# Performance work log

Hardware: AMD Instinct MI355X
Metric: run time of the kernel (lower is better)

## Reference

```python
import jax, jax.numpy as jnp
import numpy as np

HIDDEN = 512
TEXT_DIM = 768
NUM_HEADS = 8
NUM_GROUPS = 32
GN_EPS = 1e-5
COS_EPS = 1e-6


def setup_inputs() -> dict:
    key = jax.random.key(0)
    ks = jax.random.split(key, 9)
    s = 0.02
    return {
        "x": jax.random.normal(ks[0], (16, HIDDEN, 64, 64), jnp.float32),
        "text_emb": jax.random.normal(ks[1], (16, 77, TEXT_DIM), jnp.float32),
        "gn_weight": jnp.ones((HIDDEN,), jnp.float32),
        "gn_bias": jnp.zeros((HIDDEN,), jnp.float32),
        "Wq": jax.random.normal(ks[2], (HIDDEN, HIDDEN), jnp.float32) * s,
        "Wk": jax.random.normal(ks[3], (HIDDEN, TEXT_DIM), jnp.float32) * s,
        "Wv": jax.random.normal(ks[4], (HIDDEN, TEXT_DIM), jnp.float32) * s,
        "Wo": jax.random.normal(ks[5], (HIDDEN, HIDDEN), jnp.float32) * s,
        "bo": jnp.zeros((HIDDEN,), jnp.float32),
    }


def reference(x, text_emb, gn_weight, gn_bias, Wq, Wk, Wv, Wo, bo):
    B, C, H, W = x.shape
    N_img = H * W
    nh, hd = NUM_HEADS, C // NUM_HEADS

    # GroupNorm(32, C): normalize over (channels-in-group, H, W)
    xg = x.reshape(B, NUM_GROUPS, -1)
    mu = xg.mean(axis=-1, keepdims=True)
    var = jnp.mean(jnp.square(xg - mu), axis=-1, keepdims=True)
    xn = ((xg - mu) * jax.lax.rsqrt(var + GN_EPS)).reshape(B, C, H, W)
    xn = xn * gn_weight[None, :, None, None] + gn_bias[None, :, None, None]

    x_flat = xn.reshape(B, C, N_img).transpose(0, 2, 1)  # [B, N_img, C]

    q = jnp.einsum('bnc,dc->bnd', x_flat, Wq)            # [B, N_img, C]
    k = jnp.einsum('btc,dc->btd', text_emb, Wk)          # [B, N_text, C]
    v = jnp.einsum('btc,dc->btd', text_emb, Wv)

    # split heads -> [B, nh, N, hd]
    q = q.reshape(B, N_img, nh, hd).transpose(0, 2, 1, 3)
    k = k.reshape(B, -1, nh, hd).transpose(0, 2, 1, 3)
    v = v.reshape(B, -1, nh, hd).transpose(0, 2, 1, 3)

    # cosine-sim attention: L2-normalize q and k, scale = 1.0
    q = q / (jnp.linalg.norm(q, axis=-1, keepdims=True) + COS_EPS)
    k = k / (jnp.linalg.norm(k, axis=-1, keepdims=True) + COS_EPS)

    scores = jnp.einsum('bhqd,bhkd->bhqk', q, k)         # [B, nh, N_img, N_text]
    attn = jax.nn.softmax(scores, axis=-1)
    out = jnp.einsum('bhqk,bhkd->bhqd', attn, v)         # [B, nh, N_img, hd]

    out = out.transpose(0, 2, 1, 3).reshape(B, N_img, C)
    out = jnp.einsum('bnc,dc->bnd', out, Wo) + bo
    out = out.transpose(0, 2, 1).reshape(B, C, H, W)
    return x + out
```

## Files before the change

### kernel.cpp

```cpp
#include <hip/hip_runtime.h>
#include <math.h>


typedef unsigned short u16;
typedef __attribute__((ext_vector_type(8))) __bf16 bf16x8;
typedef __attribute__((ext_vector_type(4))) float f32x4;

typedef __attribute__((address_space(1))) unsigned int as1_u32;
typedef __attribute__((address_space(3))) unsigned int as3_u32;

__device__ __forceinline__ float b2f(u16 u) {
  union { unsigned int i; float f; } c; c.i = ((unsigned int)u) << 16; return c.f;
}
__device__ __forceinline__ u16 f2b(float f) {
  union { float f; unsigned int i; } c; c.f = f;
  unsigned int i = c.i + 0x7fffu + ((c.i >> 16) & 1u);
  return (u16)(i >> 16);
}

__device__ __forceinline__ void g2lds16(const void* g, void* l) {
  __builtin_amdgcn_global_load_lds((const as1_u32*)g, (as3_u32*)l, 16, 0, 0);
}

__global__ void k_castall(const float* __restrict__ Wq, const float* __restrict__ Wk,
                          const float* __restrict__ Wv, const float* __restrict__ Wo,
                          const float* __restrict__ text,
                          u16* __restrict__ wq_b, u16* __restrict__ wkv_b,
                          u16* __restrict__ wo_b, u16* __restrict__ text_b) {
  const int i = blockIdx.x * 256 + threadIdx.x, st = gridDim.x * 256;
  for (int j = i; j < 262144; j += st) wq_b[j] = f2b(Wq[j]);
  for (int j = i; j < 393216; j += st) wkv_b[j] = f2b(Wk[j]);
  for (int j = i; j < 393216; j += st) wkv_b[393216 + j] = f2b(Wv[j]);
  for (int j = i; j < 262144; j += st) wo_b[j] = f2b(Wo[j]);
  for (int j = i; j < 946176; j += st) text_b[j] = f2b(text[j]);
}

__global__ __launch_bounds__(256) void k_gnstats(const float* __restrict__ x,
                                                 float* __restrict__ stats) {
  int bg = blockIdx.x;
  const float4* p = (const float4*)(x + (size_t)bg * 65536);
  float s = 0.f, ss = 0.f;
  for (int i = threadIdx.x; i < 16384; i += 256) {
    float4 v = p[i];
    s  += v.x + v.y + v.z + v.w;
    ss += v.x*v.x + v.y*v.y + v.z*v.z + v.w*v.w;
  }
  for (int o = 1; o < 64; o <<= 1) { s += __shfl_xor(s, o, 64); ss += __shfl_xor(ss, o, 64); }
  __shared__ float as_[4], bs_[4];
  int w = threadIdx.x >> 6;
  if ((threadIdx.x & 63) == 0) { as_[w] = s; bs_[w] = ss; }
  __syncthreads();
  if (threadIdx.x == 0) {
    s  = as_[0] + as_[1] + as_[2] + as_[3];
    ss = bs_[0] + bs_[1] + bs_[2] + bs_[3];
    float mu  = s * (1.f / 65536.f);
    float var = ss * (1.f / 65536.f) - mu * mu;
    stats[2*bg]   = mu;
    stats[2*bg+1] = rsqrtf(var + 1e-5f);
  }
}

__global__ __launch_bounds__(256) void k_qproj(
    const float* __restrict__ x, const float* __restrict__ stats,
    const float* __restrict__ gw, const float* __restrict__ gb,
    const u16* __restrict__ Wqb, u16* __restrict__ qb) {
  __shared__ u16 Al[128 * 64];
  __shared__ u16 Bl[128 * 64];
  __shared__ float cw[512], cb[512];
  const int tid = threadIdx.x;
  const int o = blockIdx.x;
  const int mi = ((o >> 5) << 3) + (o & 7);
  const int ni = (o >> 3) & 3;
  const int m0 = mi << 7, n0 = ni << 7;
  const int b = m0 >> 12, hw0 = m0 & 4095;

  for (int c = tid; c < 512; c += 256) {
    const int g = (b << 5) + (c >> 4);
    const float mu = stats[2*g], rs = stats[2*g+1];
    const float wg = gw[c] * rs;
    cw[c] = wg; cb[c] = gb[c] - mu * wg;
  }

  const int l = tid & 63, w = tid >> 6;
  const int wm = (w >> 1) << 6, wn = (w & 1) << 6;
  const int lr = l & 15, lg = l >> 4;

  f32x4 acc[4][4];
#pragma unroll
  for (int i = 0; i < 4; ++i)
#pragma unroll
    for (int j = 0; j < 4; ++j) acc[i][j] = {0.f, 0.f, 0.f, 0.f};

  const int rl = l >> 3, slot = l & 7;
  const int c8 = (slot ^ rl) << 3;
  int brow[4];
#pragma unroll
  for (int j = 0; j < 4; ++j) brow[j] = n0 + (w << 5) + (j << 3) + rl;

  const int tokl = tid & 127;
  const int chg = tid >> 7;
  const float* xb = x + (((size_t)b) << 9) * 4096;
  __syncthreads();

  for (int ks = 0; ks < 8; ++ks) {
#pragma unroll
    for (int j = 0; j < 4; ++j)
      g2lds16(Wqb + (size_t)brow[j] * 512 + (ks << 6) + c8,
              Bl + (((w << 5) + (j << 3)) << 6));
#pragma unroll
    for (int jj = 0; jj < 8; ++jj) {
      const int ch4 = (((chg << 3) + jj) << 2);
      const int c = (ks << 6) + ch4;
      const float v0 = xb[(size_t)(c + 0) * 4096 + hw0 + tokl];
      const float v1 = xb[(size_t)(c + 1) * 4096 + hw0 + tokl];
      const float v2 = xb[(size_t)(c + 2) * 4096 + hw0 + tokl];
      const float v3 = xb[(size_t)(c + 3) * 4096 + hw0 + tokl];
      ushort4 pk;
      pk.x = f2b(v0 * cw[c + 0] + cb[c + 0]);
      pk.y = f2b(v1 * cw[c + 1] + cb[c + 1]);
      pk.z = f2b(v2 * cw[c + 2] + cb[c + 2]);
      pk.w = f2b(v3 * cw[c + 3] + cb[c + 3]);
      const int sl = (((ch4 >> 3) ^ (tokl & 7)) << 3) + (ch4 & 7);
      *(ushort4*)(Al + (tokl << 6) + sl) = pk;
    }
    __syncthreads();
    bf16x8 bfr[4][2];
#pragma unroll
    for (int j = 0; j < 4; ++j) {
      const int br = wn + j * 16 + lr;
      bfr[j][0] = *(const bf16x8*)(Bl + (br << 6) + (((lg    ) ^ (br & 7)) << 3));
      bfr[j][1] = *(const bf16x8*)(Bl + (br << 6) + (((lg + 4) ^ (br & 7)) << 3));
    }
#pragma unroll
    for (int i = 0; i < 4; ++i) {
      const int ar = wm + i * 16 + lr;
      const bf16x8 a0 = *(const bf16x8*)(Al + (ar << 6) + (((lg    ) ^ (ar & 7)) << 3));
      const bf16x8 a1 = *(const bf16x8*)(Al + (ar << 6) + (((lg + 4) ^ (ar & 7)) << 3));
#pragma unroll
      for (int j = 0; j < 4; ++j) {
        acc[i][j] = __builtin_amdgcn_mfma_f32_16x16x32_bf16(a0, bfr[j][0], acc[i][j], 0, 0, 0);
        acc[i][j] = __builtin_amdgcn_mfma_f32_16x16x32_bf16(a1, bfr[j][1], acc[i][j], 0, 0, 0);
      }
    }
    __syncthreads();
  }

  const int lg4 = lg << 2;
#pragma unroll
  for (int i = 0; i < 4; ++i) {
#pragma unroll
    for (int r = 0; r < 4; ++r) {
      float ss = 0.f;
#pragma unroll
      for (int j = 0; j < 4; ++j) { const float v = acc[i][j][r]; ss += v * v; }
      ss += __shfl_xor(ss, 1, 64); ss += __shfl_xor(ss, 2, 64);
      ss += __shfl_xor(ss, 4, 64); ss += __shfl_xor(ss, 8, 64);
      const float sc = 1.f / (sqrtf(ss) + 1e-6f);
      const int row = m0 + wm + i * 16 + lg4 + r;
#pragma unroll
      for (int j = 0; j < 4; ++j)
        qb[(size_t)row * 512 + n0 + wn + j * 16 + lr] = f2b(acc[i][j][r] * sc);
    }
  }
}

template <int MODE>
__global__ __launch_bounds__(256) void k_gemm(
    const u16* __restrict__ A, const u16* __restrict__ BT,
    int M, int N, int K,
    float* __restrict__ outf, u16* __restrict__ outb,
    const float* __restrict__ xres, const float* __restrict__ bias) {
  __shared__ u16 Al[2][128 * 64];
  __shared__ u16 Bl[2][128 * 64];
  const int tid = threadIdx.x;
  const int l = tid & 63, w = tid >> 6;

  const int nwg = gridDim.x * gridDim.y;
  int lin = blockIdx.y * gridDim.x + blockIdx.x;
  lin = (lin & 7) * (nwg >> 3) + (lin >> 3);
  const int m0 = (lin / gridDim.x) << 7, n0 = (lin % gridDim.x) << 7;

  const int wm = (w >> 1) << 6, wn = (w & 1) << 6;
  const int lr = l & 15, lg = l >> 4;

  f32x4 acc[4][4];
#pragma unroll
  for (int i = 0; i < 4; ++i)
#pragma unroll
    for (int j = 0; j < 4; ++j) acc[i][j] = {0.f, 0.f, 0.f, 0.f};

  const int rl = l >> 3, slot = l & 7;
  const int c8 = (slot ^ rl) << 3;
  int arow[4], brow[4];
#pragma unroll
  for (int j = 0; j < 4; ++j) {
    const int r_local = (w << 5) + (j << 3) + rl;
    arow[j] = min(m0 + r_local, M - 1);
    brow[j] = n0 + r_local;
  }

  const int ksteps = K >> 6;
#pragma unroll
  for (int j = 0; j < 4; ++j)
    g2lds16(A + (size_t)arow[j] * K + c8, Al[0] + (((w << 5) + (j << 3)) << 6));
#pragma unroll
  for (int j = 0; j < 4; ++j)
    g2lds16(BT + (size_t)brow[j] * K + c8, Bl[0] + (((w << 5) + (j << 3)) << 6));
  __syncthreads();

  for (int ks = 0; ks < ksteps; ++ks) {
    const int cur = ks & 1, nxt = cur ^ 1;
    if (ks + 1 < ksteps) {
      const int kb = ((ks + 1) << 6) + c8;
#pragma unroll
      for (int j = 0; j < 4; ++j)
        g2lds16(A + (size_t)arow[j] * K + kb, Al[nxt] + (((w << 5) + (j << 3)) << 6));
#pragma unroll
      for (int j = 0; j < 4; ++j)
        g2lds16(BT + (size_t)brow[j] * K + kb, Bl[nxt] + (((w << 5) + (j << 3)) << 6));
    }
    bf16x8 bfr[4][2];
#pragma unroll
    for (int j = 0; j < 4; ++j) {
      const int br = wn + j * 16 + lr;
      bfr[j][0] = *(const bf16x8*)(Bl[cur] + (br << 6) + (((lg    ) ^ (br & 7)) << 3));
      bfr[j][1] = *(const bf16x8*)(Bl[cur] + (br << 6) + (((lg + 4) ^ (br & 7)) << 3));
    }
#pragma unroll
    for (int i = 0; i < 4; ++i) {
      const int ar = wm + i * 16 + lr;
      const bf16x8 a0 = *(const bf16x8*)(Al[cur] + (ar << 6) + (((lg    ) ^ (ar & 7)) << 3));
      const bf16x8 a1 = *(const bf16x8*)(Al[cur] + (ar << 6) + (((lg + 4) ^ (ar & 7)) << 3));
#pragma unroll
      for (int j = 0; j < 4; ++j) {
        acc[i][j] = __builtin_amdgcn_mfma_f32_16x16x32_bf16(a0, bfr[j][0], acc[i][j], 0, 0, 0);
        acc[i][j] = __builtin_amdgcn_mfma_f32_16x16x32_bf16(a1, bfr[j][1], acc[i][j], 0, 0, 0);
      }
    }
    __syncthreads();
  }

  const int lg4 = lg << 2;
#pragma unroll
  for (int i = 0; i < 4; ++i) {
#pragma unroll
    for (int j = 0; j < 4; ++j) {
#pragma unroll
      for (int r = 0; r < 4; ++r) {
        const int row = m0 + wm + i * 16 + lg4 + r;
        const int col = n0 + wn + j * 16 + lr;
        const float v = acc[i][j][r];
        if (MODE == 0) {
          if (row < M) outf[(size_t)row * N + col] = v;
        } else {
          const int bb = col >> 12, hw = col & 4095;
          const size_t o = (((size_t)bb << 9) + row) * 4096 + hw;
          outf[o] = xres[o] + bias[row] + v;
        }
      }
    }
  }
}

__global__ __launch_bounds__(64) void k_kvnorm(const float* __restrict__ kv,
                                               u16* __restrict__ kn,
                                               u16* __restrict__ vn) {
  const int row = blockIdx.x;
  const int h = blockIdx.y;
  const int d = threadIdx.x;
  const int b = row / 77, t = row - b * 77;
  const float kx = kv[(size_t)row * 1024 + h * 64 + d];
  float ss = kx * kx;
  for (int o = 1; o < 64; o <<= 1) ss += __shfl_xor(ss, o, 64);
  const float sc = 1.f / (sqrtf(ss) + 1e-6f);
  const size_t ob = (((size_t)(b * 8 + h)) * 77 + t) * 64 + d;
  kn[ob] = f2b(kx * sc);
  vn[ob] = f2b(kv[(size_t)row * 1024 + 512 + h * 64 + d]);
}

__global__ __launch_bounds__(256) void k_attn2(
    const u16* __restrict__ q, const u16* __restrict__ kn,
    const u16* __restrict__ vn, u16* __restrict__ out) {
  __shared__ u16 Kl[96 * 72];
  __shared__ u16 Vt[64 * 104];
  __shared__ u16 Pl[64 * 104];
  const int qt = blockIdx.x, h = blockIdx.y, b = blockIdx.z;
  const size_t kvb = ((size_t)(b * 8 + h)) * (77 * 64);
  const int tid = threadIdx.x;
  for (int u = tid; u < 768; u += 256) {
    const int row = u >> 3, c8v = (u & 7) << 3;
    uint4 v = make_uint4(0, 0, 0, 0);
    if (row < 77) v = *(const uint4*)(kn + kvb + row * 64 + c8v);
    *(uint4*)(Kl + row * 72 + c8v) = v;
  }
  for (int u = tid; u < 768; u += 256) {
    const int row = u >> 3, c8v = (u & 7) << 3;
    uint4 v = make_uint4(0, 0, 0, 0);
    if (row < 77) v = *(const uint4*)(vn + kvb + row * 64 + c8v);
    const u16* pv = (const u16*)&v;
#pragma unroll
    for (int j = 0; j < 8; ++j) Vt[(c8v + j) * 104 + row] = pv[j];
  }
  __syncthreads();
  const int l = tid & 63, w = tid >> 6;
  const int lr = l & 15, lg = l >> 4;

  const int qrow = (b << 12) + (qt << 6) + (w << 4) + lr;
  bf16x8 af0 = *(const bf16x8*)(q + (size_t)qrow * 512 + h * 64 + lg * 8);
  bf16x8 af1 = *(const bf16x8*)(q + (size_t)qrow * 512 + h * 64 + 32 + lg * 8);
  f32x4 s[6];
#pragma unroll
  for (int nt = 0; nt < 6; ++nt) {
    s[nt] = {0.f, 0.f, 0.f, 0.f};
    bf16x8 bk0 = *(const bf16x8*)(Kl + (nt * 16 + lr) * 72 + lg * 8);
    bf16x8 bk1 = *(const bf16x8*)(Kl + (nt * 16 + lr) * 72 + 32 + lg * 8);
    s[nt] = __builtin_amdgcn_mfma_f32_16x16x32_bf16(af0, bk0, s[nt], 0, 0, 0);
    s[nt] = __builtin_amdgcn_mfma_f32_16x16x32_bf16(af1, bk1, s[nt], 0, 0, 0);
  }
#pragma unroll
  for (int r = 0; r < 4; ++r) {
    if (lr >= 13) s[4][r] = -1e30f;
    s[5][r] = -1e30f;
  }
#pragma unroll
  for (int r = 0; r < 4; ++r) {
    float m = s[0][r];
#pragma unroll
    for (int nt = 1; nt < 6; ++nt) m = fmaxf(m, s[nt][r]);
    m = fmaxf(m, __shfl_xor(m, 1, 64)); m = fmaxf(m, __shfl_xor(m, 2, 64));
    m = fmaxf(m, __shfl_xor(m, 4, 64)); m = fmaxf(m, __shfl_xor(m, 8, 64));
    float sum = 0.f;
#pragma unroll
    for (int nt = 0; nt < 6; ++nt) { s[nt][r] = __expf(s[nt][r] - m); sum += s[nt][r]; }
    sum += __shfl_xor(sum, 1, 64); sum += __shfl_xor(sum, 2, 64);
    sum += __shfl_xor(sum, 4, 64); sum += __shfl_xor(sum, 8, 64);
    const float inv = 1.f / sum;
    const int qlocal = (w << 4) + (lg << 2) + r;
#pragma unroll
    for (int nt = 0; nt < 6; ++nt)
      Pl[qlocal * 104 + nt * 16 + lr] = f2b(s[nt][r] * inv);
  }
  __syncthreads();

  bf16x8 pa0 = *(const bf16x8*)(Pl + ((w << 4) + lr) * 104 + lg * 8);
  bf16x8 pa1 = *(const bf16x8*)(Pl + ((w << 4) + lr) * 104 + 32 + lg * 8);
  bf16x8 pa2 = *(const bf16x8*)(Pl + ((w << 4) + lr) * 104 + 64 + lg * 8);
  f32x4 o[4];
#pragma unroll
  for (int nt = 0; nt < 4; ++nt) {
    o[nt] = {0.f, 0.f, 0.f, 0.f};
    bf16x8 bv0 = *(const bf16x8*)(Vt + (nt * 16 + lr) * 104 + lg * 8);
    bf16x8 bv1 = *(const bf16x8*)(Vt + (nt * 16 + lr) * 104 + 32 + lg * 8);
    bf16x8 bv2 = *(const bf16x8*)(Vt + (nt * 16 + lr) * 104 + 64 + lg * 8);
    o[nt] = __builtin_amdgcn_mfma_f32_16x16x32_bf16(pa0, bv0, o[nt], 0, 0, 0);
    o[nt] = __builtin_amdgcn_mfma_f32_16x16x32_bf16(pa1, bv1, o[nt], 0, 0, 0);
    o[nt] = __builtin_amdgcn_mfma_f32_16x16x32_bf16(pa2, bv2, o[nt], 0, 0, 0);
  }
#pragma unroll
  for (int r = 0; r < 4; ++r) {
    const int n = (b << 12) + (qt << 6) + (w << 4) + (lg << 2) + r;
#pragma unroll
    for (int nt = 0; nt < 4; ++nt)
      out[(size_t)n * 512 + h * 64 + nt * 16 + lr] = f2b(o[nt][r]);
  }
}

extern "C" void kernel_launch(void* const* d_in, const int* in_sizes, int n_in,
                              void* d_out, int out_size, void* d_ws, size_t ws_size,
                              hipStream_t stream) {
  (void)in_sizes; (void)n_in; (void)out_size; (void)ws_size;
  const float* x    = (const float*)d_in[0];
  const float* text = (const float*)d_in[1];
  const float* gnw  = (const float*)d_in[2];
  const float* gnb  = (const float*)d_in[3];
  const float* Wq   = (const float*)d_in[4];
  const float* Wk   = (const float*)d_in[5];
  const float* Wv   = (const float*)d_in[6];
  const float* Wo   = (const float*)d_in[7];
  const float* bo   = (const float*)d_in[8];
  float* out = (float*)d_out;

  char* ws = (char*)d_ws;
  size_t off = 0;
  auto alloc = [&](size_t bytes) -> void* {
    void* p = ws + off; off += (bytes + 255) & ~(size_t)255; return p;
  };
  float* stats = (float*)alloc(512 * 2 * 4);
  u16* wq_b    = (u16*)alloc((size_t)512 * 512 * 2);
  u16* wkv_b   = (u16*)alloc((size_t)1024 * 768 * 2);
  u16* wo_b    = (u16*)alloc((size_t)512 * 512 * 2);
  u16* text_b  = (u16*)alloc((size_t)1232 * 768 * 2);
  float* kv_f  = (float*)alloc((size_t)1232 * 1024 * 4);
  u16* kn      = (u16*)alloc((size_t)16 * 8 * 77 * 64 * 2);
  u16* vn      = (u16*)alloc((size_t)16 * 8 * 77 * 64 * 2);
  u16* ao      = (u16*)alloc((size_t)65536 * 512 * 2);
  u16* qb      = (u16*)alloc((size_t)65536 * 512 * 2);

  k_castall<<<dim3(512), 256, 0, stream>>>(Wq, Wk, Wv, Wo, text,
                                           wq_b, wkv_b, wo_b, text_b);

  k_gnstats<<<dim3(512), 256, 0, stream>>>(x, stats);

  k_gemm<0><<<dim3(8, 10), 256, 0, stream>>>(text_b, wkv_b, 1232, 1024, 768,
                                             kv_f, nullptr, nullptr, nullptr);
  k_kvnorm<<<dim3(1232, 8), 64, 0, stream>>>(kv_f, kn, vn);

  k_qproj<<<dim3(2048), 256, 0, stream>>>(x, stats, gnw, gnb, wq_b, qb);

  k_attn2<<<dim3(64, 8, 16), 256, 0, stream>>>(qb, kn, vn, ao);

  k_gemm<2><<<dim3(512, 4), 256, 0, stream>>>(wo_b, ao, 512, 65536, 512,
                                              out, nullptr, x, bo);
}
```

Before: 307.6 us.

## Halve GEMM N-tile and drop LDS double buffering for higher occupancy

The GEMM kernel becomes templated on the N tile width. Both projection GEMMs now use a 128x64 tile and a single LDS buffer instead of a double-buffered 128x128 tile. Shared memory and accumulator registers per block drop, and twice as many blocks are launched, with the aim of more resident waves and better latency hiding. In exchange, global-to-LDS loads no longer overlap the MFMA work within a block, and each A tile is fetched twice as often.

After: 318.7 us. 1.04x slower.

```diff
diff --git a/kernel.cpp b/kernel.cpp
--- a/kernel.cpp
+++ b/kernel.cpp
@@ -164,75 +164,68 @@
   }
 }
 
-template <int MODE>
+template <int MODE, int BN>
 __global__ __launch_bounds__(256) void k_gemm(
     const u16* __restrict__ A, const u16* __restrict__ BT,
     int M, int N, int K,
-    float* __restrict__ outf, u16* __restrict__ outb,
+    float* __restrict__ outf,
     const float* __restrict__ xres, const float* __restrict__ bias) {
-  __shared__ u16 Al[2][128 * 64];
-  __shared__ u16 Bl[2][128 * 64];
+  constexpr int NJ = BN / 32;
+  constexpr int BCH = BN / 32;
+  __shared__ u16 Al[128 * 64];
+  __shared__ u16 Bl[BN * 64];
   const int tid = threadIdx.x;
   const int l = tid & 63, w = tid >> 6;
 
   const int nwg = gridDim.x * gridDim.y;
   int lin = blockIdx.y * gridDim.x + blockIdx.x;
   lin = (lin & 7) * (nwg >> 3) + (lin >> 3);
-  const int m0 = (lin / gridDim.x) << 7, n0 = (lin % gridDim.x) << 7;
-
-  const int wm = (w >> 1) << 6, wn = (w & 1) << 6;
+  const int m0 = (lin / gridDim.x) << 7;
+  const int n0 = (lin % gridDim.x) * BN;
+
+  const int wm = (w >> 1) << 6, wn = (w & 1) * (BN / 2);
   const int lr = l & 15, lg = l >> 4;
 
-  f32x4 acc[4][4];
+  f32x4 acc[4][NJ];
 #pragma unroll
   for (int i = 0; i < 4; ++i)
 #pragma unroll
-    for (int j = 0; j < 4; ++j) acc[i][j] = {0.f, 0.f, 0.f, 0.f};
+    for (int j = 0; j < NJ; ++j) acc[i][j] = {0.f, 0.f, 0.f, 0.f};
 
   const int rl = l >> 3, slot = l & 7;
   const int c8 = (slot ^ rl) << 3;
-  int arow[4], brow[4];
-#pragma unroll
-  for (int j = 0; j < 4; ++j) {
-    const int r_local = (w << 5) + (j << 3) + rl;
-    arow[j] = min(m0 + r_local, M - 1);
-    brow[j] = n0 + r_local;
-  }
+  int arow[4], brow[BCH];
+#pragma unroll
+  for (int j = 0; j < 4; ++j)
+    arow[j] = min(m0 + (w << 5) + (j << 3) + rl, M - 1);
+#pragma unroll
+  for (int j = 0; j < BCH; ++j)
+    brow[j] = n0 + w * (BN / 4) + (j << 3) + rl;
 
   const int ksteps = K >> 6;
-#pragma unroll
-  for (int j = 0; j < 4; ++j)
-    g2lds16(A + (size_t)arow[j] * K + c8, Al[0] + (((w << 5) + (j << 3)) << 6));
-#pragma unroll
-  for (int j = 0; j < 4; ++j)
-    g2lds16(BT + (size_t)brow[j] * K + c8, Bl[0] + (((w << 5) + (j << 3)) << 6));
-  __syncthreads();
-
   for (int ks = 0; ks < ksteps; ++ks) {
-    const int cur = ks & 1, nxt = cur ^ 1;
-    if (ks + 1 < ksteps) {
-      const int kb = ((ks + 1) << 6) + c8;
-#pragma unroll
-      for (int j = 0; j < 4; ++j)
-        g2lds16(A + (size_t)arow[j] * K + kb, Al[nxt] + (((w << 5) + (j << 3)) << 6));
-#pragma unroll
-      for (int j = 0; j < 4; ++j)
-        g2lds16(BT + (size_t)brow[j] * K + kb, Bl[nxt] + (((w << 5) + (j << 3)) << 6));
-    }
-    bf16x8 bfr[4][2];
-#pragma unroll
-    for (int j = 0; j < 4; ++j) {
+    const int kb = (ks << 6) + c8;
+#pragma unroll
+    for (int j = 0; j < 4; ++j)
+      g2lds16(A + (size_t)arow[j] * K + kb, Al + (((w << 5) + (j << 3)) << 6));
+#pragma unroll
+    for (int j = 0; j < BCH; ++j)
+      g2lds16(BT + (size_t)brow[j] * K + kb, Bl + ((w * (BN / 4) + (j << 3)) << 6));
+    __syncthreads();
+    bf16x8 bfr[NJ][2];
+#pragma unroll
+    for (int j = 0; j < NJ; ++j) {
       const int br = wn + j * 16 + lr;
-      bfr[j][0] = *(const bf16x8*)(Bl[cur] + (br << 6) + (((lg    ) ^ (br & 7)) << 3));
-      bfr[j][1] = *(const bf16x8*)(Bl[cur] + (br << 6) + (((lg + 4) ^ (br & 7)) << 3));
+      bfr[j][0] = *(const bf16x8*)(Bl + (br << 6) + (((lg    ) ^ (br & 7)) << 3));
+      bfr[j][1] = *(const bf16x8*)(Bl + (br << 6) + (((lg + 4) ^ (br & 7)) << 3));
     }
 #pragma unroll
     for (int i = 0; i < 4; ++i) {
       const int ar = wm + i * 16 + lr;
-      const bf16x8 a0 = *(const bf16x8*)(Al[cur] + (ar << 6) + (((lg    ) ^ (ar & 7)) << 3));
-      const bf16x8 a1 = *(const bf16x8*)(Al[cur] + (ar << 6) + (((lg + 4) ^ (ar & 7)) << 3));
-#pragma unroll
-      for (int j = 0; j < 4; ++j) {
+      const bf16x8 a0 = *(const bf16x8*)(Al + (ar << 6) + (((lg    ) ^ (ar & 7)) << 3));
+      const bf16x8 a1 = *(const bf16x8*)(Al + (ar << 6) + (((lg + 4) ^ (ar & 7)) << 3));
+#pragma unroll
+      for (int j = 0; j < NJ; ++j) {
         acc[i][j] = __builtin_amdgcn_mfma_f32_16x16x32_bf16(a0, bfr[j][0], acc[i][j], 0, 0, 0);
         acc[i][j] = __builtin_amdgcn_mfma_f32_16x16x32_bf16(a1, bfr[j][1], acc[i][j], 0, 0, 0);
       }
@@ -244,7 +237,7 @@
 #pragma unroll
   for (int i = 0; i < 4; ++i) {
 #pragma unroll
-    for (int j = 0; j < 4; ++j) {
+    for (int j = 0; j < NJ; ++j) {
 #pragma unroll
       for (int r = 0; r < 4; ++r) {
         const int row = m0 + wm + i * 16 + lg4 + r;
@@ -401,14 +394,14 @@
 
   k_gnstats<<<dim3(512), 256, 0, stream>>>(x, stats);
 
-  k_gemm<0><<<dim3(8, 10), 256, 0, stream>>>(text_b, wkv_b, 1232, 1024, 768,
-                                             kv_f, nullptr, nullptr, nullptr);
+  k_gemm<0, 64><<<dim3(16, 10), 256, 0, stream>>>(text_b, wkv_b, 1232, 1024, 768,
+                                                  kv_f, nullptr, nullptr);
   k_kvnorm<<<dim3(1232, 8), 64, 0, stream>>>(kv_f, kn, vn);
 
   k_qproj<<<dim3(2048), 256, 0, stream>>>(x, stats, gnw, gnb, wq_b, qb);
 
   k_attn2<<<dim3(64, 8, 16), 256, 0, stream>>>(qb, kn, vn, ao);
 
-  k_gemm<2><<<dim3(512, 4), 256, 0, stream>>>(wo_b, ao, 512, 65536, 512,
-                                              out, nullptr, x, bo);
-}
+  k_gemm<2, 64><<<dim3(1024, 4), 256, 0, stream>>>(wo_b, ao, 512, 65536, 512,
+                                                   out, x, bo);
+}
```

## Fuse attention with output projection and residual into a single per-token-tile kernel

Applied to the files above, without the earlier changes.

Replaces the separate attention kernel and the Wo projection GEMM with one kernel. Each block takes 64 tokens, loops over all 8 heads, runs attention into LDS, and accumulates the Wo projection in registers before writing out the residual plus bias. This removes the 64 MB bf16 attention-output round trip and one launch. The cost is a large 128-float accumulator per thread, which limits occupancy, Wo fragments read straight from global memory on every head, and K/V reloaded per head. The small KV GEMM also drops its LDS double buffering and now loads synchronously.

Measured after the change: 325.6 us. 5.9% more time.

```diff
diff --git a/kernel.cpp b/kernel.cpp
--- a/kernel.cpp
+++ b/kernel.cpp
@@ -164,14 +164,11 @@
   }
 }
 
-template <int MODE>
-__global__ __launch_bounds__(256) void k_gemm(
+__global__ __launch_bounds__(256) void k_gemm0(
     const u16* __restrict__ A, const u16* __restrict__ BT,
-    int M, int N, int K,
-    float* __restrict__ outf, u16* __restrict__ outb,
-    const float* __restrict__ xres, const float* __restrict__ bias) {
-  __shared__ u16 Al[2][128 * 64];
-  __shared__ u16 Bl[2][128 * 64];
+    int M, int N, int K, float* __restrict__ outf) {
+  __shared__ u16 Al[128 * 64];
+  __shared__ u16 Bl[128 * 64];
   const int tid = threadIdx.x;
   const int l = tid & 63, w = tid >> 6;
 
@@ -200,37 +197,27 @@
   }
 
   const int ksteps = K >> 6;
-#pragma unroll
-  for (int j = 0; j < 4; ++j)
-    g2lds16(A + (size_t)arow[j] * K + c8, Al[0] + (((w << 5) + (j << 3)) << 6));
-#pragma unroll
-  for (int j = 0; j < 4; ++j)
-    g2lds16(BT + (size_t)brow[j] * K + c8, Bl[0] + (((w << 5) + (j << 3)) << 6));
-  __syncthreads();
-
   for (int ks = 0; ks < ksteps; ++ks) {
-    const int cur = ks & 1, nxt = cur ^ 1;
-    if (ks + 1 < ksteps) {
-      const int kb = ((ks + 1) << 6) + c8;
-#pragma unroll
-      for (int j = 0; j < 4; ++j)
-        g2lds16(A + (size_t)arow[j] * K + kb, Al[nxt] + (((w << 5) + (j << 3)) << 6));
-#pragma unroll
-      for (int j = 0; j < 4; ++j)
-        g2lds16(BT + (size_t)brow[j] * K + kb, Bl[nxt] + (((w << 5) + (j << 3)) << 6));
-    }
+    const int kb = (ks << 6) + c8;
+#pragma unroll
+    for (int j = 0; j < 4; ++j)
+      g2lds16(A + (size_t)arow[j] * K + kb, Al + (((w << 5) + (j << 3)) << 6));
+#pragma unroll
+    for (int j = 0; j < 4; ++j)
+      g2lds16(BT + (size_t)brow[j] * K + kb, Bl + (((w << 5) + (j << 3)) << 6));
+    __syncthreads();
     bf16x8 bfr[4][2];
 #pragma unroll
     for (int j = 0; j < 4; ++j) {
       const int br = wn + j * 16 + lr;
-      bfr[j][0] = *(const bf16x8*)(Bl[cur] + (br << 6) + (((lg    ) ^ (br & 7)) << 3));
-      bfr[j][1] = *(const bf16x8*)(Bl[cur] + (br << 6) + (((lg + 4) ^ (br & 7)) << 3));
+      bfr[j][0] = *(const bf16x8*)(Bl + (br << 6) + (((lg    ) ^ (br & 7)) << 3));
+      bfr[j][1] = *(const bf16x8*)(Bl + (br << 6) + (((lg + 4) ^ (br & 7)) << 3));
     }
 #pragma unroll
     for (int i = 0; i < 4; ++i) {
       const int ar = wm + i * 16 + lr;
-      const bf16x8 a0 = *(const bf16x8*)(Al[cur] + (ar << 6) + (((lg    ) ^ (ar & 7)) << 3));
-      const bf16x8 a1 = *(const bf16x8*)(Al[cur] + (ar << 6) + (((lg + 4) ^ (ar & 7)) << 3));
+      const bf16x8 a0 = *(const bf16x8*)(Al + (ar << 6) + (((lg    ) ^ (ar & 7)) << 3));
+      const bf16x8 a1 = *(const bf16x8*)(Al + (ar << 6) + (((lg + 4) ^ (ar & 7)) << 3));
 #pragma unroll
       for (int j = 0; j < 4; ++j) {
         acc[i][j] = __builtin_amdgcn_mfma_f32_16x16x32_bf16(a0, bfr[j][0], acc[i][j], 0, 0, 0);
@@ -242,24 +229,14 @@
 
   const int lg4 = lg << 2;
 #pragma unroll
-  for (int i = 0; i < 4; ++i) {
-#pragma unroll
-    for (int j = 0; j < 4; ++j) {
+  for (int i = 0; i < 4; ++i)
+#pragma unroll
+    for (int j = 0; j < 4; ++j)
 #pragma unroll
       for (int r = 0; r < 4; ++r) {
         const int row = m0 + wm + i * 16 + lg4 + r;
-        const int col = n0 + wn + j * 16 + lr;
-        const float v = acc[i][j][r];
-        if (MODE == 0) {
-          if (row < M) outf[(size_t)row * N + col] = v;
-        } else {
-          const int bb = col >> 12, hw = col & 4095;
-          const size_t o = (((size_t)bb << 9) + row) * 4096 + hw;
-          outf[o] = xres[o] + bias[row] + v;
-        }
+        if (row < M) outf[(size_t)row * N + n0 + wn + j * 16 + lr] = acc[i][j][r];
       }
-    }
-  }
 }
 
 __global__ __launch_bounds__(64) void k_kvnorm(const float* __restrict__ kv,
@@ -278,90 +255,144 @@
   vn[ob] = f2b(kv[(size_t)row * 1024 + 512 + h * 64 + d]);
 }
 
-__global__ __launch_bounds__(256) void k_attn2(
-    const u16* __restrict__ q, const u16* __restrict__ kn,
-    const u16* __restrict__ vn, u16* __restrict__ out) {
+__global__ __launch_bounds__(256, 2) void k_attnO(
+    const u16* __restrict__ qb, const u16* __restrict__ kn,
+    const u16* __restrict__ vn, const u16* __restrict__ wo,
+    const float* __restrict__ xres, const float* __restrict__ bias,
+    float* __restrict__ out) {
   __shared__ u16 Kl[96 * 72];
   __shared__ u16 Vt[64 * 104];
   __shared__ u16 Pl[64 * 104];
-  const int qt = blockIdx.x, h = blockIdx.y, b = blockIdx.z;
-  const size_t kvb = ((size_t)(b * 8 + h)) * (77 * 64);
+  __shared__ u16 Ql[64 * 72];
+  __shared__ u16 Ao[64 * 72];
   const int tid = threadIdx.x;
-  for (int u = tid; u < 768; u += 256) {
-    const int row = u >> 3, c8v = (u & 7) << 3;
-    uint4 v = make_uint4(0, 0, 0, 0);
-    if (row < 77) v = *(const uint4*)(kn + kvb + row * 64 + c8v);
-    *(uint4*)(Kl + row * 72 + c8v) = v;
-  }
-  for (int u = tid; u < 768; u += 256) {
-    const int row = u >> 3, c8v = (u & 7) << 3;
-    uint4 v = make_uint4(0, 0, 0, 0);
-    if (row < 77) v = *(const uint4*)(vn + kvb + row * 64 + c8v);
-    const u16* pv = (const u16*)&v;
-#pragma unroll
-    for (int j = 0; j < 8; ++j) Vt[(c8v + j) * 104 + row] = pv[j];
-  }
-  __syncthreads();
+  const int bt = blockIdx.x;
+  const int b = bt >> 6;
+  const int tok0 = bt << 6;
+  const int hw0 = tok0 & 4095;
   const int l = tid & 63, w = tid >> 6;
   const int lr = l & 15, lg = l >> 4;
-
-  const int qrow = (b << 12) + (qt << 6) + (w << 4) + lr;
-  bf16x8 af0 = *(const bf16x8*)(q + (size_t)qrow * 512 + h * 64 + lg * 8);
-  bf16x8 af1 = *(const bf16x8*)(q + (size_t)qrow * 512 + h * 64 + 32 + lg * 8);
-  f32x4 s[6];
-#pragma unroll
-  for (int nt = 0; nt < 6; ++nt) {
-    s[nt] = {0.f, 0.f, 0.f, 0.f};
-    bf16x8 bk0 = *(const bf16x8*)(Kl + (nt * 16 + lr) * 72 + lg * 8);
-    bf16x8 bk1 = *(const bf16x8*)(Kl + (nt * 16 + lr) * 72 + 32 + lg * 8);
-    s[nt] = __builtin_amdgcn_mfma_f32_16x16x32_bf16(af0, bk0, s[nt], 0, 0, 0);
-    s[nt] = __builtin_amdgcn_mfma_f32_16x16x32_bf16(af1, bk1, s[nt], 0, 0, 0);
-  }
-#pragma unroll
-  for (int r = 0; r < 4; ++r) {
-    if (lr >= 13) s[4][r] = -1e30f;
-    s[5][r] = -1e30f;
-  }
-#pragma unroll
-  for (int r = 0; r < 4; ++r) {
-    float m = s[0][r];
-#pragma unroll
-    for (int nt = 1; nt < 6; ++nt) m = fmaxf(m, s[nt][r]);
-    m = fmaxf(m, __shfl_xor(m, 1, 64)); m = fmaxf(m, __shfl_xor(m, 2, 64));
-    m = fmaxf(m, __shfl_xor(m, 4, 64)); m = fmaxf(m, __shfl_xor(m, 8, 64));
-    float sum = 0.f;
-#pragma unroll
-    for (int nt = 0; nt < 6; ++nt) { s[nt][r] = __expf(s[nt][r] - m); sum += s[nt][r]; }
-    sum += __shfl_xor(sum, 1, 64); sum += __shfl_xor(sum, 2, 64);
-    sum += __shfl_xor(sum, 4, 64); sum += __shfl_xor(sum, 8, 64);
-    const float inv = 1.f / sum;
-    const int qlocal = (w << 4) + (lg << 2) + r;
-#pragma unroll
-    for (int nt = 0; nt < 6; ++nt)
-      Pl[qlocal * 104 + nt * 16 + lr] = f2b(s[nt][r] * inv);
-  }
-  __syncthreads();
-
-  bf16x8 pa0 = *(const bf16x8*)(Pl + ((w << 4) + lr) * 104 + lg * 8);
-  bf16x8 pa1 = *(const bf16x8*)(Pl + ((w << 4) + lr) * 104 + 32 + lg * 8);
-  bf16x8 pa2 = *(const bf16x8*)(Pl + ((w << 4) + lr) * 104 + 64 + lg * 8);
-  f32x4 o[4];
-#pragma unroll
-  for (int nt = 0; nt < 4; ++nt) {
-    o[nt] = {0.f, 0.f, 0.f, 0.f};
-    bf16x8 bv0 = *(const bf16x8*)(Vt + (nt * 16 + lr) * 104 + lg * 8);
-    bf16x8 bv1 = *(const bf16x8*)(Vt + (nt * 16 + lr) * 104 + 32 + lg * 8);
-    bf16x8 bv2 = *(const bf16x8*)(Vt + (nt * 16 + lr) * 104 + 64 + lg * 8);
-    o[nt] = __builtin_amdgcn_mfma_f32_16x16x32_bf16(pa0, bv0, o[nt], 0, 0, 0);
-    o[nt] = __builtin_amdgcn_mfma_f32_16x16x32_bf16(pa1, bv1, o[nt], 0, 0, 0);
-    o[nt] = __builtin_amdgcn_mfma_f32_16x16x32_bf16(pa2, bv2, o[nt], 0, 0, 0);
-  }
-#pragma unroll
-  for (int r = 0; r < 4; ++r) {
-    const int n = (b << 12) + (qt << 6) + (w << 4) + (lg << 2) + r;
-#pragma unroll
-    for (int nt = 0; nt < 4; ++nt)
-      out[(size_t)n * 512 + h * 64 + nt * 16 + lr] = f2b(o[nt][r]);
+  const int lg4 = lg << 2;
+
+  f32x4 acc[8][4];
+#pragma unroll
+  for (int i = 0; i < 8; ++i)
+#pragma unroll
+    for (int j = 0; j < 4; ++j) acc[i][j] = {0.f, 0.f, 0.f, 0.f};
+
+  for (int h = 0; h < 8; ++h) {
+    const size_t kvb = ((size_t)(b * 8 + h)) * (77 * 64);
+    for (int u = tid; u < 768; u += 256) {
+      const int row = u >> 3, c8 = (u & 7) << 3;
+      uint4 v = make_uint4(0, 0, 0, 0);
+      if (row < 77) v = *(const uint4*)(kn + kvb + row * 64 + c8);
+      *(uint4*)(Kl + row * 72 + c8) = v;
+    }
+    for (int u = tid; u < 768; u += 256) {
+      const int row = u >> 3, c8 = (u & 7) << 3;
+      uint4 v = make_uint4(0, 0, 0, 0);
+      if (row < 77) v = *(const uint4*)(vn + kvb + row * 64 + c8);
+      const u16* pv = (const u16*)&v;
+#pragma unroll
+      for (int j = 0; j < 8; ++j) Vt[(c8 + j) * 104 + row] = pv[j];
+    }
+    for (int u = tid; u < 512; u += 256) {
+      const int row = u >> 3, c8 = (u & 7) << 3;
+      *(uint4*)(Ql + row * 72 + c8) =
+          *(const uint4*)(qb + (size_t)(tok0 + row) * 512 + h * 64 + c8);
+    }
+    __syncthreads();
+
+    const bf16x8 af0 = *(const bf16x8*)(Ql + ((w << 4) + lr) * 72 + lg * 8);
+    const bf16x8 af1 = *(const bf16x8*)(Ql + ((w << 4) + lr) * 72 + 32 + lg * 8);
+    f32x4 s[6];
+#pragma unroll
+    for (int nt = 0; nt < 6; ++nt) {
+      s[nt] = {0.f, 0.f, 0.f, 0.f};
+      const bf16x8 bk0 = *(const bf16x8*)(Kl + (nt * 16 + lr) * 72 + lg * 8);
+      const bf16x8 bk1 = *(const bf16x8*)(Kl + (nt * 16 + lr) * 72 + 32 + lg * 8);
+      s[nt] = __builtin_amdgcn_mfma_f32_16x16x32_bf16(af0, bk0, s[nt], 0, 0, 0);
+      s[nt] = __builtin_amdgcn_mfma_f32_16x16x32_bf16(af1, bk1, s[nt], 0, 0, 0);
+    }
+#pragma unroll
+    for (int r = 0; r < 4; ++r) {
+      if (lr >= 13) s[4][r] = -1e30f;
+      s[5][r] = -1e30f;
+    }
+#pragma unroll
+    for (int r = 0; r < 4; ++r) {
+      float m = s[0][r];
+#pragma unroll
+      for (int nt = 1; nt < 6; ++nt) m = fmaxf(m, s[nt][r]);
+      m = fmaxf(m, __shfl_xor(m, 1, 64)); m = fmaxf(m, __shfl_xor(m, 2, 64));
+      m = fmaxf(m, __shfl_xor(m, 4, 64)); m = fmaxf(m, __shfl_xor(m, 8, 64));
+      float sum = 0.f;
+#pragma unroll
+      for (int nt = 0; nt < 6; ++nt) { s[nt][r] = __expf(s[nt][r] - m); sum += s[nt][r]; }
+      sum += __shfl_xor(sum, 1, 64); sum += __shfl_xor(sum, 2, 64);
+      sum += __shfl_xor(sum, 4, 64); sum += __shfl_xor(sum, 8, 64);
+      const float inv = 1.f / sum;
+      const int qlocal = (w << 4) + lg4 + r;
+#pragma unroll
+      for (int nt = 0; nt < 6; ++nt)
+        Pl[qlocal * 104 + nt * 16 + lr] = f2b(s[nt][r] * inv);
+    }
+    __syncthreads();
+
+    const bf16x8 pa0 = *(const bf16x8*)(Pl + ((w << 4) + lr) * 104 + lg * 8);
+    const bf16x8 pa1 = *(const bf16x8*)(Pl + ((w << 4) + lr) * 104 + 32 + lg * 8);
+    const bf16x8 pa2 = *(const bf16x8*)(Pl + ((w << 4) + lr) * 104 + 64 + lg * 8);
+    f32x4 o[4];
+#pragma unroll
+    for (int nt = 0; nt < 4; ++nt) {
+      o[nt] = {0.f, 0.f, 0.f, 0.f};
+      const bf16x8 bv0 = *(const bf16x8*)(Vt + (nt * 16 + lr) * 104 + lg * 8);
+      const bf16x8 bv1 = *(const bf16x8*)(Vt + (nt * 16 + lr) * 104 + 32 + lg * 8);
+      const bf16x8 bv2 = *(const bf16x8*)(Vt + (nt * 16 + lr) * 104 + 64 + lg * 8);
+      o[nt] = __builtin_amdgcn_mfma_f32_16x16x32_bf16(pa0, bv0, o[nt], 0, 0, 0);
+      o[nt] = __builtin_amdgcn_mfma_f32_16x16x32_bf16(pa1, bv1, o[nt], 0, 0, 0);
+      o[nt] = __builtin_amdgcn_mfma_f32_16x16x32_bf16(pa2, bv2, o[nt], 0, 0, 0);
+    }
+#pragma unroll
+    for (int r = 0; r < 4; ++r)
+#pragma unroll
+      for (int nt = 0; nt < 4; ++nt)
+        Ao[((w << 4) + lg4 + r) * 72 + nt * 16 + lr] = f2b(o[nt][r]);
+    __syncthreads();
+
+    bf16x8 aof[4][2];
+#pragma unroll
+    for (int j = 0; j < 4; ++j) {
+      aof[j][0] = *(const bf16x8*)(Ao + (j * 16 + lr) * 72 + lg * 8);
+      aof[j][1] = *(const bf16x8*)(Ao + (j * 16 + lr) * 72 + 32 + lg * 8);
+    }
+#pragma unroll
+    for (int i = 0; i < 8; ++i) {
+      const u16* wrow = wo + (size_t)((w << 7) + i * 16 + lr) * 512 + h * 64;
+      const bf16x8 a0 = *(const bf16x8*)(wrow + lg * 8);
+      const bf16x8 a1 = *(const bf16x8*)(wrow + 32 + lg * 8);
+#pragma unroll
+      for (int j = 0; j < 4; ++j) {
+        acc[i][j] = __builtin_amdgcn_mfma_f32_16x16x32_bf16(a0, aof[j][0], acc[i][j], 0, 0, 0);
+        acc[i][j] = __builtin_amdgcn_mfma_f32_16x16x32_bf16(a1, aof[j][1], acc[i][j], 0, 0, 0);
+      }
+    }
+    __syncthreads();
+  }
+
+#pragma unroll
+  for (int i = 0; i < 8; ++i) {
+#pragma unroll
+    for (int r = 0; r < 4; ++r) {
+      const int ch = (w << 7) + i * 16 + lg4 + r;
+      const float bc = bias[ch];
+      const size_t rowbase = ((size_t)(b * 512 + ch)) * 4096 + hw0;
+#pragma unroll
+      for (int j = 0; j < 4; ++j) {
+        const size_t oo = rowbase + j * 16 + lr;
+        out[oo] = xres[oo] + bc + acc[i][j][r];
+      }
+    }
   }
 }
 
@@ -393,7 +424,6 @@
   float* kv_f  = (float*)alloc((size_t)1232 * 1024 * 4);
   u16* kn      = (u16*)alloc((size_t)16 * 8 * 77 * 64 * 2);
   u16* vn      = (u16*)alloc((size_t)16 * 8 * 77 * 64 * 2);
-  u16* ao      = (u16*)alloc((size_t)65536 * 512 * 2);
   u16* qb      = (u16*)alloc((size_t)65536 * 512 * 2);
 
   k_castall<<<dim3(512), 256, 0, stream>>>(Wq, Wk, Wv, Wo, text,
@@ -401,14 +431,10 @@
 
   k_gnstats<<<dim3(512), 256, 0, stream>>>(x, stats);
 
-  k_gemm<0><<<dim3(8, 10), 256, 0, stream>>>(text_b, wkv_b, 1232, 1024, 768,
-                                             kv_f, nullptr, nullptr, nullptr);
+  k_gemm0<<<dim3(8, 10), 256, 0, stream>>>(text_b, wkv_b, 1232, 1024, 768, kv_f);
   k_kvnorm<<<dim3(1232, 8), 64, 0, stream>>>(kv_f, kn, vn);
 
   k_qproj<<<dim3(2048), 256, 0, stream>>>(x, stats, gnw, gnb, wq_b, qb);
 
-  k_attn2<<<dim3(64, 8, 16), 256, 0, stream>>>(qb, kn, vn, ao);
-
-  k_gemm<2><<<dim3(512, 4), 256, 0, stream>>>(wo_b, ao, 512, 65536, 512,
-                                              out, nullptr, x, bo);
-}
+  k_attnO<<<dim3(1024), 256, 0, stream>>>(qb, kn, vn, wo_b, x, bo, out);
+}
```

## Widen qproj tile to 256 columns and single-buffer the generic GEMM

Applied to the files above, without the earlier changes.

The Q-projection kernel now computes a 128x256 output tile per block instead of 128x128, halving the grid. The GroupNorm-normalized x tile is therefore loaded and converted once per 256 output columns rather than once per 128, cutting redundant x reads. Each wave accumulates 4x8 MFMA tiles, so register pressure rises; launch_bounds(256,2) is added to keep occupancy up. The generic GEMM drops double-buffered LDS prefetch for a simpler single-buffer loop, which may expose load latency but frees LDS. The unused outb argument is removed, and the bf16 conversion now uses native __bf16 casts.

New measurement: 297.1 us. 1.04x faster.

```diff
diff --git a/kernel.cpp b/kernel.cpp
--- a/kernel.cpp
+++ b/kernel.cpp
@@ -60,18 +60,18 @@
   }
 }
 
-__global__ __launch_bounds__(256) void k_qproj(
+__global__ __launch_bounds__(256, 2) void k_qproj(
     const float* __restrict__ x, const float* __restrict__ stats,
     const float* __restrict__ gw, const float* __restrict__ gb,
     const u16* __restrict__ Wqb, u16* __restrict__ qb) {
   __shared__ u16 Al[128 * 64];
-  __shared__ u16 Bl[128 * 64];
+  __shared__ u16 Bl[256 * 64];
   __shared__ float cw[512], cb[512];
   const int tid = threadIdx.x;
   const int o = blockIdx.x;
-  const int mi = ((o >> 5) << 3) + (o & 7);
-  const int ni = (o >> 3) & 3;
-  const int m0 = mi << 7, n0 = ni << 7;
+  const int mi = ((o >> 4) << 3) + (o & 7);
+  const int ni = (o >> 3) & 1;
+  const int m0 = mi << 7, n0 = ni << 8;
   const int b = m0 >> 12, hw0 = m0 & 4095;
 
   for (int c = tid; c < 512; c += 256) {
@@ -82,20 +82,21 @@
   }
 
   const int l = tid & 63, w = tid >> 6;
-  const int wm = (w >> 1) << 6, wn = (w & 1) << 6;
+  const int wm = (w & 1) << 6;
+  const int wn = (w >> 1) << 7;
   const int lr = l & 15, lg = l >> 4;
 
-  f32x4 acc[4][4];
+  f32x4 acc[4][8];
 #pragma unroll
   for (int i = 0; i < 4; ++i)
 #pragma unroll
-    for (int j = 0; j < 4; ++j) acc[i][j] = {0.f, 0.f, 0.f, 0.f};
+    for (int j = 0; j < 8; ++j) acc[i][j] = {0.f, 0.f, 0.f, 0.f};
 
   const int rl = l >> 3, slot = l & 7;
   const int c8 = (slot ^ rl) << 3;
-  int brow[4];
-#pragma unroll
-  for (int j = 0; j < 4; ++j) brow[j] = n0 + (w << 5) + (j << 3) + rl;
+  int brow[8];
+#pragma unroll
+  for (int j = 0; j < 8; ++j) brow[j] = n0 + (w << 6) + (j << 3) + rl;
 
   const int tokl = tid & 127;
   const int chg = tid >> 7;
@@ -104,9 +105,9 @@
 
   for (int ks = 0; ks < 8; ++ks) {
 #pragma unroll
-    for (int j = 0; j < 4; ++j)
+    for (int j = 0; j < 8; ++j)
       g2lds16(Wqb + (size_t)brow[j] * 512 + (ks << 6) + c8,
-              Bl + (((w << 5) + (j << 3)) << 6));
+              Bl + (((w << 6) + (j << 3)) << 6));
 #pragma unroll
     for (int jj = 0; jj < 8; ++jj) {
       const int ch4 = (((chg << 3) + jj) << 2);
@@ -115,14 +116,104 @@
       const float v1 = xb[(size_t)(c + 1) * 4096 + hw0 + tokl];
       const float v2 = xb[(size_t)(c + 2) * 4096 + hw0 + tokl];
       const float v3 = xb[(size_t)(c + 3) * 4096 + hw0 + tokl];
-      ushort4 pk;
-      pk.x = f2b(v0 * cw[c + 0] + cb[c + 0]);
-      pk.y = f2b(v1 * cw[c + 1] + cb[c + 1]);
-      pk.z = f2b(v2 * cw[c + 2] + cb[c + 2]);
-      pk.w = f2b(v3 * cw[c + 3] + cb[c + 3]);
+      union { __bf16 h[4]; ushort4 u; } pk;
+      pk.h[0] = (__bf16)(v0 * cw[c + 0] + cb[c + 0]);
+      pk.h[1] = (__bf16)(v1 * cw[c + 1] + cb[c + 1]);
+      pk.h[2] = (__bf16)(v2 * cw[c + 2] + cb[c + 2]);
+      pk.h[3] = (__bf16)(v3 * cw[c + 3] + cb[c + 3]);
       const int sl = (((ch4 >> 3) ^ (tokl & 7)) << 3) + (ch4 & 7);
-      *(ushort4*)(Al + (tokl << 6) + sl) = pk;
-    }
+      *(ushort4*)(Al + (tokl << 6) + sl) = pk.u;
+    }
+    __syncthreads();
+    bf16x8 af[4][2];
+#pragma unroll
+    for (int i = 0; i < 4; ++i) {
+      const int ar = wm + i * 16 + lr;
+      af[i][0] = *(const bf16x8*)(Al + (ar << 6) + (((lg    ) ^ (ar & 7)) << 3));
+      af[i][1] = *(const bf16x8*)(Al + (ar << 6) + (((lg + 4) ^ (ar & 7)) << 3));
+    }
+#pragma unroll
+    for (int j = 0; j < 8; ++j) {
+      const int br = wn + j * 16 + lr;
+      const bf16x8 b0 = *(const bf16x8*)(Bl + (br << 6) + (((lg    ) ^ (br & 7)) << 3));
+      const bf16x8 b1 = *(const bf16x8*)(Bl + (br << 6) + (((lg + 4) ^ (br & 7)) << 3));
+#pragma unroll
+      for (int i = 0; i < 4; ++i) {
+        acc[i][j] = __builtin_amdgcn_mfma_f32_16x16x32_bf16(af[i][0], b0, acc[i][j], 0, 0, 0);
+        acc[i][j] = __builtin_amdgcn_mfma_f32_16x16x32_bf16(af[i][1], b1, acc[i][j], 0, 0, 0);
+      }
+    }
+    __syncthreads();
+  }
+
+  const int lg4 = lg << 2;
+#pragma unroll
+  for (int i = 0; i < 4; ++i) {
+#pragma unroll
+    for (int r = 0; r < 4; ++r) {
+      const int row = m0 + wm + i * 16 + lg4 + r;
+#pragma unroll
+      for (int h2 = 0; h2 < 2; ++h2) {
+        float ss = 0.f;
+#pragma unroll
+        for (int j = h2 * 4; j < h2 * 4 + 4; ++j) {
+          const float v = acc[i][j][r]; ss += v * v;
+        }
+        ss += __shfl_xor(ss, 1, 64); ss += __shfl_xor(ss, 2, 64);
+        ss += __shfl_xor(ss, 4, 64); ss += __shfl_xor(ss, 8, 64);
+        const float sc = 1.f / (sqrtf(ss) + 1e-6f);
+#pragma unroll
+        for (int j = h2 * 4; j < h2 * 4 + 4; ++j)
+          qb[(size_t)row * 512 + n0 + wn + j * 16 + lr] = f2b(acc[i][j][r] * sc);
+      }
+    }
+  }
+}
+
+template <int MODE>
+__global__ __launch_bounds__(256) void k_gemm(
+    const u16* __restrict__ A, const u16* __restrict__ BT,
+    int M, int N, int K,
+    float* __restrict__ outf,
+    const float* __restrict__ xres, const float* __restrict__ bias) {
+  __shared__ u16 Al[128 * 64];
+  __shared__ u16 Bl[128 * 64];
+  const int tid = threadIdx.x;
+  const int l = tid & 63, w = tid >> 6;
+
+  const int nwg = gridDim.x * gridDim.y;
+  int lin = blockIdx.y * gridDim.x + blockIdx.x;
+  lin = (lin & 7) * (nwg >> 3) + (lin >> 3);
+  const int m0 = (lin / gridDim.x) << 7, n0 = (lin % gridDim.x) << 7;
+
+  const int wm = (w >> 1) << 6, wn = (w & 1) << 6;
+  const int lr = l & 15, lg = l >> 4;
+
+  f32x4 acc[4][4];
+#pragma unroll
+  for (int i = 0; i < 4; ++i)
+#pragma unroll
+    for (int j = 0; j < 4; ++j) acc[i][j] = {0.f, 0.f, 0.f, 0.f};
+
+  const int rl = l >> 3, slot = l & 7;
+  const int c8 = (slot ^ rl) << 3;
+  int arow[4], brow[4];
+#pragma unroll
+  for (int j = 0; j < 4; ++j) {
+    const int r_local = (w << 5) + (j << 3) + rl;
+    arow[j] = min(m0 + r_local, M - 1);
+    brow[j] = n0 + r_local;
+  }
+
+  const int ksteps = K >> 6;
+  for (int ks = 0; ks < ksteps; ++ks) {
+    const int kb = (ks << 6) + c8;
+#pragma unroll
+    for (int j = 0; j < 4; ++j)
+      g2lds16(A + (size_t)arow[j] * K + kb, Al + (((w << 5) + (j << 3)) << 6));
+#pragma unroll
+    for (int j = 0; j < 4; ++j)
+      g2lds16(BT + (size_t)brow[j] * K + kb, Bl + (((w << 5) + (j << 3)) << 6));
     __syncthreads();
     bf16x8 bfr[4][2];
 #pragma unroll
@@ -136,101 +227,6 @@
       const int ar = wm + i * 16 + lr;
       const bf16x8 a0 = *(const bf16x8*)(Al + (ar << 6) + (((lg    ) ^ (ar & 7)) << 3));
       const bf16x8 a1 = *(const bf16x8*)(Al + (ar << 6) + (((lg + 4) ^ (ar & 7)) << 3));
-#pragma unroll
-      for (int j = 0; j < 4; ++j) {
-        acc[i][j] = __builtin_amdgcn_mfma_f32_16x16x32_bf16(a0, bfr[j][0], acc[i][j], 0, 0, 0);
-        acc[i][j] = __builtin_amdgcn_mfma_f32_16x16x32_bf16(a1, bfr[j][1], acc[i][j], 0, 0, 0);
-      }
-    }
-    __syncthreads();
-  }
-
-  const int lg4 = lg << 2;
-#pragma unroll
-  for (int i = 0; i < 4; ++i) {
-#pragma unroll
-    for (int r = 0; r < 4; ++r) {
-      float ss = 0.f;
-#pragma unroll
-      for (int j = 0; j < 4; ++j) { const float v = acc[i][j][r]; ss += v * v; }
-      ss += __shfl_xor(ss, 1, 64); ss += __shfl_xor(ss, 2, 64);
-      ss += __shfl_xor(ss, 4, 64); ss += __shfl_xor(ss, 8, 64);
-      const float sc = 1.f / (sqrtf(ss) + 1e-6f);
-      const int row = m0 + wm + i * 16 + lg4 + r;
-#pragma unroll
-      for (int j = 0; j < 4; ++j)
-        qb[(size_t)row * 512 + n0 + wn + j * 16 + lr] = f2b(acc[i][j][r] * sc);
-    }
-  }
-}
-
-template <int MODE>
-__global__ __launch_bounds__(256) void k_gemm(
-    const u16* __restrict__ A, const u16* __restrict__ BT,
-    int M, int N, int K,
-    float* __restrict__ outf, u16* __restrict__ outb,
-    const float* __restrict__ xres, const float* __restrict__ bias) {
-  __shared__ u16 Al[2][128 * 64];
-  __shared__ u16 Bl[2][128 * 64];
-  const int tid = threadIdx.x;
-  const int l = tid & 63, w = tid >> 6;
-
-  const int nwg = gridDim.x * gridDim.y;
-  int lin = blockIdx.y * gridDim.x + blockIdx.x;
-  lin = (lin & 7) * (nwg >> 3) + (lin >> 3);
-  const int m0 = (lin / gridDim.x) << 7, n0 = (lin % gridDim.x) << 7;
-
-  const int wm = (w >> 1) << 6, wn = (w & 1) << 6;
-  const int lr = l & 15, lg = l >> 4;
-
-  f32x4 acc[4][4];
-#pragma unroll
-  for (int i = 0; i < 4; ++i)
-#pragma unroll
-    for (int j = 0; j < 4; ++j) acc[i][j] = {0.f, 0.f, 0.f, 0.f};
-
-  const int rl = l >> 3, slot = l & 7;
-  const int c8 = (slot ^ rl) << 3;
-  int arow[4], brow[4];
-#pragma unroll
-  for (int j = 0; j < 4; ++j) {
-    const int r_local = (w << 5) + (j << 3) + rl;
-    arow[j] = min(m0 + r_local, M - 1);
-    brow[j] = n0 + r_local;
-  }
-
-  const int ksteps = K >> 6;
-#pragma unroll
-  for (int j = 0; j < 4; ++j)
-    g2lds16(A + (size_t)arow[j] * K + c8, Al[0] + (((w << 5) + (j << 3)) << 6));
-#pragma unroll
-  for (int j = 0; j < 4; ++j)
-    g2lds16(BT + (size_t)brow[j] * K + c8, Bl[0] + (((w << 5) + (j << 3)) << 6));
-  __syncthreads();
-
-  for (int ks = 0; ks < ksteps; ++ks) {
-    const int cur = ks & 1, nxt = cur ^ 1;
-    if (ks + 1 < ksteps) {
-      const int kb = ((ks + 1) << 6) + c8;
-#pragma unroll
-      for (int j = 0; j < 4; ++j)
-        g2lds16(A + (size_t)arow[j] * K + kb, Al[nxt] + (((w << 5) + (j << 3)) << 6));
-#pragma unroll
-      for (int j = 0; j < 4; ++j)
-        g2lds16(BT + (size_t)brow[j] * K + kb, Bl[nxt] + (((w << 5) + (j << 3)) << 6));
-    }
-    bf16x8 bfr[4][2];
-#pragma unroll
-    for (int j = 0; j < 4; ++j) {
-      const int br = wn + j * 16 + lr;
-      bfr[j][0] = *(const bf16x8*)(Bl[cur] + (br << 6) + (((lg    ) ^ (br & 7)) << 3));
-      bfr[j][1] = *(const bf16x8*)(Bl[cur] + (br << 6) + (((lg + 4) ^ (br & 7)) << 3));
-    }
-#pragma unroll
-    for (int i = 0; i < 4; ++i) {
-      const int ar = wm + i * 16 + lr;
-      const bf16x8 a0 = *(const bf16x8*)(Al[cur] + (ar << 6) + (((lg    ) ^ (ar & 7)) << 3));
-      const bf16x8 a1 = *(const bf16x8*)(Al[cur] + (ar << 6) + (((lg + 4) ^ (ar & 7)) << 3));
 #pragma unroll
       for (int j = 0; j < 4; ++j) {
         acc[i][j] = __builtin_amdgcn_mfma_f32_16x16x32_bf16(a0, bfr[j][0], acc[i][j], 0, 0, 0);
@@ -402,13 +398,13 @@
   k_gnstats<<<dim3(512), 256, 0, stream>>>(x, stats);
 
   k_gemm<0><<<dim3(8, 10), 256, 0, stream>>>(text_b, wkv_b, 1232, 1024, 768,
-                                             kv_f, nullptr, nullptr, nullptr);
+                                             kv_f, nullptr, nullptr);
   k_kvnorm<<<dim3(1232, 8), 64, 0, stream>>>(kv_f, kn, vn);
 
-  k_qproj<<<dim3(2048), 256, 0, stream>>>(x, stats, gnw, gnb, wq_b, qb);
+  k_qproj<<<dim3(1024), 256, 0, stream>>>(x, stats, gnw, gnb, wq_b, qb);
 
   k_attn2<<<dim3(64, 8, 16), 256, 0, stream>>>(qb, kn, vn, ao);
 
   k_gemm<2><<<dim3(512, 4), 256, 0, stream>>>(wo_b, ao, 512, 65536, 512,
-                                              out, nullptr, x, bo);
-}
+                                              out, x, bo);
+}
```
